# Kernel tuning notes

Measured on AMD Instinct MI355X. Metric: run time of the kernel, lower is better.

The kernel has to match this reference:

```python
import jax, jax.numpy as jnp
import numpy as np
import math

HID = 128      # hidden_dim == d_inner (expand=1)
NSTATE = 8     # d_state
K = 4          # scan directions
RANK = math.ceil(HID / 16)  # dt_rank = 8
B, H, W = 4, 64, 64


def _ln(x, g, b, eps=1e-5):
    m = jnp.mean(x, -1, keepdims=True)
    v = jnp.mean((x - m) ** 2, -1, keepdims=True)
    return (x - m) * jax.lax.rsqrt(v + eps) * g + b


def _ss2d(x, in_w, conv_w, conv_b, xproj_w, dt_w, dt_b, A_logs, Ds, ln_g, ln_b, out_w):
    # x: [B,H,W,C] -> VMamba SS2D with d_inner=C, 4-direction selective scan
    Bn, Hh, Ww, C = x.shape
    D, L = C, Hh * Ww
    N = A_logs.shape[-1]
    R = dt_w.shape[-1]
    xz = x @ in_w.T                      # [B,H,W,2D]
    xc, z = jnp.split(xz, 2, axis=-1)
    xc = xc.transpose(0, 3, 1, 2)        # [B,D,H,W]
    xc = jax.lax.conv_general_dilated(xc, conv_w, (1, 1), 'SAME', feature_group_count=D)
    xc = jax.nn.silu(xc + conv_b[None, :, None, None])
    x_hw = xc.reshape(Bn, D, L)
    x_wh = xc.transpose(0, 1, 3, 2).reshape(Bn, D, L)
    xs = jnp.stack([x_hw, x_wh, x_hw[..., ::-1], x_wh[..., ::-1]], 1)  # [B,K,D,L]
    x_dbl = jnp.einsum('bkdl,kcd->bkcl', xs, xproj_w)
    dts, Bs, Cs = x_dbl[:, :, :R], x_dbl[:, :, R:R + N], x_dbl[:, :, R + N:]
    dt = jax.nn.softplus(jnp.einsum('bkrl,kdr->bkdl', dts, dt_w) + dt_b[None, :, :, None])
    A = -jnp.exp(A_logs.reshape(K, D, N))  # [K,D,N]

    def step(h, inp):
        x_t, dt_t, B_t, C_t = inp          # [B,K,D],[B,K,D],[B,K,N],[B,K,N]
        h = h * jnp.exp(dt_t[..., None] * A) + dt_t[..., None] * B_t[:, :, None, :] * x_t[..., None]
        return h, jnp.einsum('bkdn,bkn->bkd', h, C_t)

    h0 = jnp.zeros((Bn, K, D, N), x.dtype)
    _, ys = jax.lax.scan(step, h0, (xs.transpose(3, 0, 1, 2), dt.transpose(3, 0, 1, 2),
                                    Bs.transpose(3, 0, 1, 2), Cs.transpose(3, 0, 1, 2)))
    out_y = ys.transpose(1, 2, 3, 0) + Ds.reshape(K, D)[None, :, :, None] * xs  # [B,K,D,L]
    wh_y = out_y[:, 3, :, ::-1].reshape(Bn, D, Ww, Hh).transpose(0, 1, 3, 2).reshape(Bn, D, L)
    invwh_y = out_y[:, 1].reshape(Bn, D, Ww, Hh).transpose(0, 1, 3, 2).reshape(Bn, D, L)
    y = out_y[:, 0] + out_y[:, 2, :, ::-1] + wh_y + invwh_y
    y = _ln(y.transpose(0, 2, 1).reshape(Bn, Hh, Ww, D), ln_g, ln_b)
    return (y * jax.nn.silu(z)) @ out_w.T


def _enhance(x, g, b, w, bias):
    return jax.nn.gelu(_ln(x, g, b) @ w.T + bias, approximate=False)


def setup_inputs() -> dict:
    key = jax.random.key(0)
    ks = jax.random.split(key, 12)
    f = lambda k, s, sc=0.02: jax.random.normal(k, s, jnp.float32) * sc
    return dict(
        sar_feat=jax.random.normal(ks[0], (B, H, W, HID), jnp.float32),
        opt_feat=jax.random.normal(ks[1], (B, H, W, HID), jnp.float32),
        ss_in_w=f(ks[2], (2, 2 * HID, HID)),
        ss_conv_w=f(ks[3], (2, HID, 1, 3, 3), 0.1),
        ss_conv_b=f(ks[4], (2, HID)),
        ss_xproj_w=f(ks[5], (2, K, RANK + 2 * NSTATE, HID)),
        ss_dt_w=f(ks[6], (2, K, HID, RANK), 0.1),
        ss_dt_b=f(ks[7], (2, K, HID), 0.1),
        ss_Alogs=jnp.tile(jnp.log(jnp.arange(1, NSTATE + 1, dtype=jnp.float32)), (2, K * HID, 1)),
        ss_Ds=jnp.ones((2, K * HID), jnp.float32),
        ss_ln_g=jnp.ones((2, HID), jnp.float32),
        ss_ln_b=jnp.zeros((2, HID), jnp.float32),
        ss_out_w=f(ks[8], (2, HID, HID)),
        enh_ln_g=jnp.ones((2, HID), jnp.float32),
        enh_ln_b=jnp.zeros((2, HID), jnp.float32),
        enh_w=f(ks[9], (2, HID, HID)),
        enh_b=jnp.zeros((2, HID), jnp.float32),
    )


def reference(sar_feat, opt_feat, ss_in_w, ss_conv_w, ss_conv_b, ss_xproj_w, ss_dt_w,
              ss_dt_b, ss_Alogs, ss_Ds, ss_ln_g, ss_ln_b, ss_out_w,
              enh_ln_g, enh_ln_b, enh_w, enh_b):
    # cat([opt,sar],-1)[...,:C] == opt ; cat([sar,opt],-1)[...,:C] == sar (faithful identity slice)
    # index 0 = cross_ss2d_s2o (input opt), index 1 = cross_ss2d_o2s (input sar)
    xin = jnp.stack([opt_feat, sar_feat])
    guided = jax.vmap(_ss2d)(xin, ss_in_w, ss_conv_w, ss_conv_b, ss_xproj_w, ss_dt_w,
                             ss_dt_b, ss_Alogs, ss_Ds, ss_ln_g, ss_ln_b, ss_out_w)
    # enhance params: index 0 = enhance_sar (on sar_guided=guided[1]), index 1 = enhance_opt (on opt_guided=guided[0])
    enh_in = jnp.stack([guided[1], guided[0]])
    enhanced = jax.vmap(_enhance)(enh_in, enh_ln_g, enh_ln_b, enh_w, enh_b)
    return (sar_feat + enhanced[0], opt_feat + enhanced[1])
```

## Files before the change

kernel.cpp:

```cpp
#include <hip/hip_runtime.h>
#include <hip/hip_bf16.h>
#include <math.h>

#define DEV __device__ __forceinline__

static constexpr int LL = 4096;
static constexpr int DD = 128;
static constexpr int SEG = 64;
static constexpr float LOG2E = 1.4426950408889634f;
static constexpr float LN2 = 0.6931471805599453f;

template <bool B> struct BoolT { static constexpr bool value = B; };

DEV float silu_(float x) { return x / (1.f + __expf(-x)); }
DEV float gelu_(float x) { return 0.5f * x * (1.f + erff(x * 0.7071067811865475f)); }
DEV float sp_(float x) {
  const float t = __builtin_amdgcn_exp2f(-fabsf(x) * LOG2E);
  return fmaxf(x, 0.f) + LN2 * __builtin_amdgcn_logf(1.f + t);
}

template <int CTRL>
DEV float dpp_add_(float x) {
  int y = __builtin_amdgcn_update_dpp(0, __float_as_int(x), CTRL, 0xF, 0xF, true);
  return x + __int_as_float(y);
}

DEV void seg_base_step(int k, int s, int& base, int& step) {
  if (k == 0)      { base = s * 64;        step = 1;   }
  else if (k == 1) { base = s;             step = 64;  }
  else if (k == 2) { base = 4095 - s * 64; step = -1;  }
  else             { base = 4095 - s;      step = -64; }
}

__global__ __launch_bounds__(256) void k_inproj(
    const float* __restrict__ sar, const float* __restrict__ opt,
    const float* __restrict__ in_w, float* __restrict__ xz) {
  const int lt = blockIdx.x, ct = blockIdx.y, mb = blockIdx.z;
  const int m = mb >> 2;
  const float* __restrict__ x = (m == 0 ? opt : sar) + (size_t)(mb & 3) * (LL * DD);
  const float* __restrict__ W = in_w + (size_t)m * 256 * DD;
  __shared__ float sA[64][68];
  __shared__ float sW[64][68];
  const int tid = threadIdx.x;
  const int tc = tid & 15, tl = tid >> 4;
  float acc[4][4] = {};
  for (int db = 0; db < 2; ++db) {
    __syncthreads();
    for (int idx = tid; idx < 64 * 16; idx += 256) {
      const int r = idx >> 4, d4 = (idx & 15) << 2;
      *(float4*)&sA[r][d4] = *(const float4*)&x[(size_t)(lt * 64 + r) * DD + db * 64 + d4];
      *(float4*)&sW[r][d4] = *(const float4*)&W[(size_t)(ct * 64 + r) * DD + db * 64 + d4];
    }
    __syncthreads();
#pragma unroll 4
    for (int d = 0; d < 64; d += 4) {
      float4 a[4], w[4];
#pragma unroll
      for (int q = 0; q < 4; ++q) a[q] = *(const float4*)&sA[tl * 4 + q][d];
#pragma unroll
      for (int j = 0; j < 4; ++j) w[j] = *(const float4*)&sW[tc + 16 * j][d];
#pragma unroll
      for (int j = 0; j < 4; ++j)
#pragma unroll
        for (int q = 0; q < 4; ++q)
          acc[j][q] += a[q].x * w[j].x + a[q].y * w[j].y + a[q].z * w[j].z + a[q].w * w[j].w;
    }
  }
  float* __restrict__ dst = xz + ((size_t)mb * 256 + ct * 64) * LL + lt * 64;
#pragma unroll
  for (int j = 0; j < 4; ++j) {
    float4 v = make_float4(acc[j][0], acc[j][1], acc[j][2], acc[j][3]);
    *(float4*)&dst[(size_t)(tc + 16 * j) * LL + tl * 4] = v;
  }
}

__global__ __launch_bounds__(256) void k_conv(
    const float* __restrict__ xz, const float* __restrict__ conv_w,
    const float* __restrict__ conv_b, float* __restrict__ xc) {
  const int ht = blockIdx.x, dg = blockIdx.y, mb = blockIdx.z;
  const int m = mb >> 2;
  __shared__ float sIn[8][18][66];
  __shared__ float sOut[1024][8];
  const float* __restrict__ src = xz + ((size_t)mb * 256 + dg * 8) * LL;
  const int tid = threadIdx.x;
  for (int idx = tid; idx < 8 * 18 * 66; idx += 256) {
    const int dd = idx / (18 * 66);
    const int rem = idx - dd * (18 * 66);
    const int hh = rem / 66, ww = rem - hh * 66;
    const int h = ht * 16 + hh - 1, w = ww - 1;
    float v = 0.f;
    if (h >= 0 && h < 64 && w >= 0 && w < 64) v = src[(size_t)dd * LL + h * 64 + w];
    sIn[dd][hh][ww] = v;
  }
  __syncthreads();
  const int dd = tid & 7, wv = tid >> 3;
  const int dch = dg * 8 + dd;
  float wk[9];
#pragma unroll
  for (int t = 0; t < 9; ++t) wk[t] = conv_w[((size_t)m * DD + dch) * 9 + t];
  const float bias = conv_b[m * DD + dch];
  for (int hh = 0; hh < 16; ++hh) {
#pragma unroll
    for (int wh = 0; wh < 2; ++wh) {
      const int w = wv + wh * 32;
      float s = bias;
#pragma unroll
      for (int kh = 0; kh < 3; ++kh)
#pragma unroll
        for (int kw = 0; kw < 3; ++kw)
          s = fmaf(sIn[dd][hh + kh][w + kw], wk[kh * 3 + kw], s);
      sOut[hh * 64 + w][dd] = silu_(s);
    }
  }
  __syncthreads();
  float* __restrict__ dst = xc + (size_t)mb * LL * DD + dg * 8;
#pragma unroll
  for (int r = 0; r < 4; ++r) {
    const int pos = tid + r * 256;
    const int l = ht * 1024 + pos;
    *(float4*)&dst[(size_t)l * DD + 0] = *(const float4*)&sOut[pos][0];
    *(float4*)&dst[(size_t)l * DD + 4] = *(const float4*)&sOut[pos][4];
  }
}

__global__ __launch_bounds__(256) void k_xproj(
    const float* __restrict__ xc, const float* __restrict__ xproj_w,
    float* __restrict__ xdbl) {
  const int lt = blockIdx.x, k = blockIdx.y, mb = blockIdx.z;
  const int m = mb >> 2, mbk = mb * 4 + k;
  __shared__ float sX[64][132];
  __shared__ float sW[24][132];
  const int tid = threadIdx.x;
  const float* __restrict__ src = xc + (size_t)mb * LL * DD;
  int base, step;
  seg_base_step(k, lt, base, step);
  for (int idx = tid; idx < 64 * 32; idx += 256) {
    const int l = idx >> 5, d4 = (idx & 31) << 2;
    *(float4*)&sX[l][d4] = *(const float4*)&src[(size_t)(base + l * step) * DD + d4];
  }
  const float* __restrict__ Wsrc = xproj_w + ((size_t)m * 4 + k) * 24 * DD;
  for (int idx = tid; idx < 24 * 32; idx += 256) {
    const int r = idx >> 5, d4 = (idx & 31) << 2;
    *(float4*)&sW[r][d4] = *(const float4*)&Wsrc[(size_t)r * DD + d4];
  }
  __syncthreads();
  const int l = tid >> 2, cg = tid & 3;
  float acc[6] = {};
#pragma unroll 8
  for (int d = 0; d < 128; d += 4) {
    const float4 xv = *(const float4*)&sX[l][d];
#pragma unroll
    for (int j = 0; j < 6; ++j) {
      const float4 wv = *(const float4*)&sW[cg * 6 + j][d];
      acc[j] += xv.x * wv.x + xv.y * wv.y + xv.z * wv.z + xv.w * wv.w;
    }
  }
  float* __restrict__ dst = xdbl + ((size_t)mbk * LL + lt * 64 + l) * 24 + cg * 6;
#pragma unroll
  for (int j = 0; j < 6; ++j) dst[j] = acc[j];
}


__global__ __launch_bounds__(128) void k_scan1(
    const float* __restrict__ xc, const float* __restrict__ xdbl,
    const float* __restrict__ dt_w, const float* __restrict__ dt_b,
    const float* __restrict__ Alogs, float* __restrict__ hend,
    float* __restrict__ Pseg) {
  const int seg = blockIdx.x;
  const int k = blockIdx.y, mb = blockIdx.z;
  const int m = mb >> 2, mbk = mb * 4 + k;
  const int d = threadIdx.x;
  __shared__ float slds[64 * 24];

  float aln2[8];
  {
    const float4 a0 = *(const float4*)&Alogs[((size_t)m * 512 + k * DD + d) * 8];
    const float4 a1 = *(const float4*)&Alogs[((size_t)m * 512 + k * DD + d) * 8 + 4];
    aln2[0] = -__expf(a0.x) * LOG2E; aln2[1] = -__expf(a0.y) * LOG2E;
    aln2[2] = -__expf(a0.z) * LOG2E; aln2[3] = -__expf(a0.w) * LOG2E;
    aln2[4] = -__expf(a1.x) * LOG2E; aln2[5] = -__expf(a1.y) * LOG2E;
    aln2[6] = -__expf(a1.z) * LOG2E; aln2[7] = -__expf(a1.w) * LOG2E;
  }
  bool fastp = true;
#pragma unroll
  for (int n = 1; n < 8; ++n)
    fastp = fastp && (fabsf(aln2[n] - (float)(n + 1) * aln2[0]) <=
                      1e-4f * fabsf(aln2[n]) + 1e-12f);
  float wreg[8];
  {
    const float4 w0 = *(const float4*)&dt_w[((size_t)mbk * DD + d) * 8];
    const float4 w1 = *(const float4*)&dt_w[((size_t)mbk * DD + d) * 8 + 4];
    wreg[0] = w0.x; wreg[1] = w0.y; wreg[2] = w0.z; wreg[3] = w0.w;
    wreg[4] = w1.x; wreg[5] = w1.y; wreg[6] = w1.z; wreg[7] = w1.w;
  }
  const float bw = dt_b[(size_t)mbk * DD + d];

  const float* __restrict__ tsrc = xdbl + ((size_t)mbk * LL + seg * 64) * 24;
#pragma unroll
  for (int t = 0; t < 3; ++t) {
    const int idx = d + t * 128;
    ((float4*)slds)[idx] = ((const float4*)tsrc)[idx];
  }

  int base, step;
  seg_base_step(k, seg, base, step);
  const float* __restrict__ xsrc = xc + (size_t)mb * LL * DD + (size_t)base * DD + d;
  const ptrdiff_t sstep = (ptrdiff_t)step * DD;

  float xreg[8];
#pragma unroll
  for (int j = 0; j < 8; ++j) xreg[j] = xsrc[(ptrdiff_t)j * sstep];
  __syncthreads();

  float h[8] = {0.f, 0.f, 0.f, 0.f, 0.f, 0.f, 0.f, 0.f};
  float dtsum = 0.f;

  auto body = [&](auto ft) {
    constexpr bool F = decltype(ft)::value;
#pragma unroll
    for (int i = 0; i < 64; ++i) {
      const float x = xreg[i & 7];
      if (i + 8 < 64) xreg[i & 7] = xsrc[(ptrdiff_t)(i + 8) * sstep];
      const float4 t0 = *(const float4*)&slds[i * 24 + 0];
      const float4 t1 = *(const float4*)&slds[i * 24 + 4];
      float s = bw;
      s = fmaf(t0.x, wreg[0], s); s = fmaf(t0.y, wreg[1], s);
      s = fmaf(t0.z, wreg[2], s); s = fmaf(t0.w, wreg[3], s);
      s = fmaf(t1.x, wreg[4], s); s = fmaf(t1.y, wreg[5], s);
      s = fmaf(t1.z, wreg[6], s); s = fmaf(t1.w, wreg[7], s);
      const float dt = sp_(s);
      const float u = dt * x;
      dtsum += dt;
      float q1, q2, q3, q4, q5, q6, q7, q8;
      if constexpr (F) {
        q1 = __builtin_amdgcn_exp2f(dt * aln2[0]);
        q2 = q1 * q1; q3 = q2 * q1; q4 = q2 * q2;
        q5 = q4 * q1; q6 = q4 * q2; q7 = q4 * q3; q8 = q4 * q4;
      } else {
        q1 = __builtin_amdgcn_exp2f(dt * aln2[0]);
        q2 = __builtin_amdgcn_exp2f(dt * aln2[1]);
        q3 = __builtin_amdgcn_exp2f(dt * aln2[2]);
        q4 = __builtin_amdgcn_exp2f(dt * aln2[3]);
        q5 = __builtin_amdgcn_exp2f(dt * aln2[4]);
        q6 = __builtin_amdgcn_exp2f(dt * aln2[5]);
        q7 = __builtin_amdgcn_exp2f(dt * aln2[6]);
        q8 = __builtin_amdgcn_exp2f(dt * aln2[7]);
      }
      const float4 b0 = *(const float4*)&slds[i * 24 + 8];
      const float4 b1 = *(const float4*)&slds[i * 24 + 12];
      h[0] = fmaf(h[0], q1, u * b0.x);
      h[1] = fmaf(h[1], q2, u * b0.y);
      h[2] = fmaf(h[2], q3, u * b0.z);
      h[3] = fmaf(h[3], q4, u * b0.w);
      h[4] = fmaf(h[4], q5, u * b1.x);
      h[5] = fmaf(h[5], q6, u * b1.y);
      h[6] = fmaf(h[6], q7, u * b1.z);
      h[7] = fmaf(h[7], q8, u * b1.w);
    }
  };
  if (fastp) body(BoolT<true>{}); else body(BoolT<false>{});

  float* __restrict__ he = hend + (((size_t)mbk * SEG + seg) << 10) + d * 8;
  float* __restrict__ pe = Pseg + (((size_t)mbk * SEG + seg) << 10) + d * 8;
  *(float4*)&he[0] = make_float4(h[0], h[1], h[2], h[3]);
  *(float4*)&he[4] = make_float4(h[4], h[5], h[6], h[7]);
  *(float4*)&pe[0] = make_float4(
      __builtin_amdgcn_exp2f(aln2[0] * dtsum), __builtin_amdgcn_exp2f(aln2[1] * dtsum),
      __builtin_amdgcn_exp2f(aln2[2] * dtsum), __builtin_amdgcn_exp2f(aln2[3] * dtsum));
  *(float4*)&pe[4] = make_float4(
      __builtin_amdgcn_exp2f(aln2[4] * dtsum), __builtin_amdgcn_exp2f(aln2[5] * dtsum),
      __builtin_amdgcn_exp2f(aln2[6] * dtsum), __builtin_amdgcn_exp2f(aln2[7] * dtsum));
}

__global__ __launch_bounds__(256) void k_scan2(
    const float* __restrict__ hend, const float* __restrict__ Pseg,
    float* __restrict__ hin) {
  const int gid = blockIdx.x * 256 + threadIdx.x;
  const int mbk = gid >> 10, dn = gid & 1023;
  const float* __restrict__ P = Pseg + ((size_t)mbk << 16) + dn;
  const float* __restrict__ E = hend + ((size_t)mbk << 16) + dn;
  float* __restrict__ O = hin + ((size_t)mbk << 16) + dn;
  float h = 0.f;
#pragma unroll
  for (int s = 0; s < SEG; ++s) {
    O[(size_t)s << 10] = h;
    if (s < SEG - 1) h = fmaf(P[(size_t)s << 10], h, E[(size_t)s << 10]);
  }
}

__global__ __launch_bounds__(128) void k_scan3(
    const float* __restrict__ xc, const float* __restrict__ xdbl,
    const float* __restrict__ dt_w, const float* __restrict__ dt_b,
    const float* __restrict__ Alogs, const float* __restrict__ Ds,
    const float* __restrict__ hin, float* __restrict__ ysum) {
  const int seg = blockIdx.x;
  const int k = blockIdx.y, mb = blockIdx.z;
  const int m = mb >> 2, mbk = mb * 4 + k;
  const int d = threadIdx.x;
  __shared__ float slds[64 * 24];

  float aln2[8];
  {
    const float4 a0 = *(const float4*)&Alogs[((size_t)m * 512 + k * DD + d) * 8];
    const float4 a1 = *(const float4*)&Alogs[((size_t)m * 512 + k * DD + d) * 8 + 4];
    aln2[0] = -__expf(a0.x) * LOG2E; aln2[1] = -__expf(a0.y) * LOG2E;
    aln2[2] = -__expf(a0.z) * LOG2E; aln2[3] = -__expf(a0.w) * LOG2E;
    aln2[4] = -__expf(a1.x) * LOG2E; aln2[5] = -__expf(a1.y) * LOG2E;
    aln2[6] = -__expf(a1.z) * LOG2E; aln2[7] = -__expf(a1.w) * LOG2E;
  }
  bool fastp = true;
#pragma unroll
  for (int n = 1; n < 8; ++n)
    fastp = fastp && (fabsf(aln2[n] - (float)(n + 1) * aln2[0]) <=
                      1e-4f * fabsf(aln2[n]) + 1e-12f);
  float wreg[8];
  {
    const float4 w0 = *(const float4*)&dt_w[((size_t)mbk * DD + d) * 8];
    const float4 w1 = *(const float4*)&dt_w[((size_t)mbk * DD + d) * 8 + 4];
    wreg[0] = w0.x; wreg[1] = w0.y; wreg[2] = w0.z; wreg[3] = w0.w;
    wreg[4] = w1.x; wreg[5] = w1.y; wreg[6] = w1.z; wreg[7] = w1.w;
  }
  const float bw = dt_b[(size_t)mbk * DD + d];
  const float dsv = Ds[(size_t)m * 512 + k * DD + d];

  const float* __restrict__ tsrc = xdbl + ((size_t)mbk * LL + seg * 64) * 24;
#pragma unroll
  for (int t = 0; t < 3; ++t) {
    const int idx = d + t * 128;
    ((float4*)slds)[idx] = ((const float4*)tsrc)[idx];
  }

  int base, step;
  seg_base_step(k, seg, base, step);
  const float* __restrict__ xsrc = xc + (size_t)mb * LL * DD + (size_t)base * DD + d;
  float* __restrict__ ydst = ysum + (size_t)mb * LL * DD + (size_t)base * DD + d;
  const ptrdiff_t sstep = (ptrdiff_t)step * DD;

  float xreg[8];
#pragma unroll
  for (int j = 0; j < 8; ++j) xreg[j] = xsrc[(ptrdiff_t)j * sstep];

  float h[8];
  {
    const float* __restrict__ hp = hin + (((size_t)mbk * SEG + seg) << 10) + d * 8;
    const float4 h0 = *(const float4*)&hp[0];
    const float4 h1 = *(const float4*)&hp[4];
    h[0] = h0.x; h[1] = h0.y; h[2] = h0.z; h[3] = h0.w;
    h[4] = h1.x; h[5] = h1.y; h[6] = h1.z; h[7] = h1.w;
  }
  __syncthreads();

  auto body = [&](auto ft) {
    constexpr bool F = decltype(ft)::value;
#pragma unroll
    for (int i = 0; i < 64; ++i) {
      const float x = xreg[i & 7];
      if (i + 8 < 64) xreg[i & 7] = xsrc[(ptrdiff_t)(i + 8) * sstep];
      const float4 t0 = *(const float4*)&slds[i * 24 + 0];
      const float4 t1 = *(const float4*)&slds[i * 24 + 4];
      float s = bw;
      s = fmaf(t0.x, wreg[0], s); s = fmaf(t0.y, wreg[1], s);
      s = fmaf(t0.z, wreg[2], s); s = fmaf(t0.w, wreg[3], s);
      s = fmaf(t1.x, wreg[4], s); s = fmaf(t1.y, wreg[5], s);
      s = fmaf(t1.z, wreg[6], s); s = fmaf(t1.w, wreg[7], s);
      const float dt = sp_(s);
      const float u = dt * x;
      float q1, q2, q3, q4, q5, q6, q7, q8;
      if constexpr (F) {
        q1 = __builtin_amdgcn_exp2f(dt * aln2[0]);
        q2 = q1 * q1; q3 = q2 * q1; q4 = q2 * q2;
        q5 = q4 * q1; q6 = q4 * q2; q7 = q4 * q3; q8 = q4 * q4;
      } else {
        q1 = __builtin_amdgcn_exp2f(dt * aln2[0]);
        q2 = __builtin_amdgcn_exp2f(dt * aln2[1]);
        q3 = __builtin_amdgcn_exp2f(dt * aln2[2]);
        q4 = __builtin_amdgcn_exp2f(dt * aln2[3]);
        q5 = __builtin_amdgcn_exp2f(dt * aln2[4]);
        q6 = __builtin_amdgcn_exp2f(dt * aln2[5]);
        q7 = __builtin_amdgcn_exp2f(dt * aln2[6]);
        q8 = __builtin_amdgcn_exp2f(dt * aln2[7]);
      }
      const float4 b0 = *(const float4*)&slds[i * 24 + 8];
      const float4 b1 = *(const float4*)&slds[i * 24 + 12];
      const float4 c0 = *(const float4*)&slds[i * 24 + 16];
      const float4 c1 = *(const float4*)&slds[i * 24 + 20];
      float y = dsv * x;
      h[0] = fmaf(h[0], q1, u * b0.x); y = fmaf(h[0], c0.x, y);
      h[1] = fmaf(h[1], q2, u * b0.y); y = fmaf(h[1], c0.y, y);
      h[2] = fmaf(h[2], q3, u * b0.z); y = fmaf(h[2], c0.z, y);
      h[3] = fmaf(h[3], q4, u * b0.w); y = fmaf(h[3], c0.w, y);
      h[4] = fmaf(h[4], q5, u * b1.x); y = fmaf(h[4], c1.x, y);
      h[5] = fmaf(h[5], q6, u * b1.y); y = fmaf(h[5], c1.y, y);
      h[6] = fmaf(h[6], q7, u * b1.z); y = fmaf(h[6], c1.z, y);
      h[7] = fmaf(h[7], q8, u * b1.w); y = fmaf(h[7], c1.w, y);
      unsafeAtomicAdd(ydst + (ptrdiff_t)i * sstep, y);
    }
  };
  if (fastp) body(BoolT<true>{}); else body(BoolT<false>{});
}

__global__ __launch_bounds__(256) void k_outproj(
    const float* __restrict__ ysum, const float* __restrict__ xz,
    const float* __restrict__ ln_g, const float* __restrict__ ln_b,
    const float* __restrict__ out_w, float* __restrict__ guided) {
  const int lt = blockIdx.x, mb = blockIdx.y;
  const int m = mb >> 2;
  __shared__ float sv[32][132];
  __shared__ float sW[64][68];
  __shared__ float smr[32][2];
  __shared__ float sg[128], sb[128];
  const int tid = threadIdx.x;
  if (tid < 128) { sg[tid] = ln_g[m * DD + tid]; sb[tid] = ln_b[m * DD + tid]; }
  const float4* __restrict__ ysrc = (const float4*)(ysum + ((size_t)mb * LL + lt * 32) * DD);
  for (int idx = tid; idx < 1024; idx += 256)
    *(float4*)&sv[idx >> 5][(idx & 31) << 2] = ysrc[idx];
  __syncthreads();
  {
    const int l = tid >> 3, q = tid & 7;
    float s = 0.f, s2 = 0.f;
#pragma unroll
    for (int d0 = 0; d0 < 16; d0 += 4) {
      const float4 v = *(const float4*)&sv[l][q * 16 + d0];
      s += v.x + v.y + v.z + v.w;
      s2 += v.x * v.x + v.y * v.y + v.z * v.z + v.w * v.w;
    }
    s = dpp_add_<0xB1>(s); s = dpp_add_<0x4E>(s); s = dpp_add_<0x141>(s);
    s2 = dpp_add_<0xB1>(s2); s2 = dpp_add_<0x4E>(s2); s2 = dpp_add_<0x141>(s2);
    if (q == 0) {
      const float mean = s * (1.f / 128.f);
      smr[l][0] = mean;
      smr[l][1] = rsqrtf(fmaf(s2, 1.f / 128.f, -mean * mean) + 1e-5f);
    }
  }
  __syncthreads();
  {
    const int c = tid >> 1, half = tid & 1;
    const float* __restrict__ zsrc = xz + ((size_t)mb * 256 + 128 + c) * LL + lt * 32 + half * 16;
    const float g = sg[c], bb = sb[c];
#pragma unroll
    for (int i = 0; i < 16; i += 4) {
      const float4 z4 = *(const float4*)&zsrc[i];
      const float zz[4] = {z4.x, z4.y, z4.z, z4.w};
#pragma unroll
      for (int t = 0; t < 4; ++t) {
        const int l = half * 16 + i + t;
        const float v = fmaf((sv[l][c] - smr[l][0]) * smr[l][1], g, bb);
        sv[l][c] = v * silu_(zz[t]);
      }
    }
  }
  const int tc = tid & 15, tl = tid >> 4;
  const float* __restrict__ Wp = out_w + (size_t)m * DD * DD;
  float* __restrict__ dst = guided + ((size_t)mb * LL + lt * 32) * DD;
  for (int jb = 0; jb < 2; ++jb) {
    float acc[4][2] = {};
    for (int db = 0; db < 2; ++db) {
      __syncthreads();
      for (int idx = tid; idx < 64 * 16; idx += 256) {
        const int r = idx >> 4, d4 = (idx & 15) << 2;
        *(float4*)&sW[r][d4] = *(const float4*)&Wp[(size_t)(jb * 64 + r) * DD + db * 64 + d4];
      }
      __syncthreads();
#pragma unroll 4
      for (int d0 = 0; d0 < 64; d0 += 4) {
        float4 av[2], wv[4];
#pragma unroll
        for (int q = 0; q < 2; ++q) av[q] = *(const float4*)&sv[tl * 2 + q][db * 64 + d0];
#pragma unroll
        for (int j = 0; j < 4; ++j) wv[j] = *(const float4*)&sW[tc + 16 * j][d0];
#pragma unroll
        for (int j = 0; j < 4; ++j)
#pragma unroll
          for (int q = 0; q < 2; ++q)
            acc[j][q] += av[q].x * wv[j].x + av[q].y * wv[j].y + av[q].z * wv[j].z + av[q].w * wv[j].w;
      }
    }
#pragma unroll
    for (int j = 0; j < 4; ++j)
#pragma unroll
      for (int q = 0; q < 2; ++q)
        dst[(size_t)(tl * 2 + q) * DD + jb * 64 + tc + 16 * j] = acc[j][q];
  }
}

__global__ __launch_bounds__(256) void k_enhance(
    const float* __restrict__ guided, const float* __restrict__ eg,
    const float* __restrict__ ebv, const float* __restrict__ ew,
    const float* __restrict__ ebias, const float* __restrict__ sar,
    const float* __restrict__ opt, float* __restrict__ outp) {
  const int lt = blockIdx.x, ib = blockIdx.y;
  const int i = ib >> 2, b = ib & 3;
  __shared__ float sv[32][132];
  __shared__ float sW[64][68];
  __shared__ float smr[32][2];
  __shared__ float sg[128], sb2[128], sbias[128];
  const int tid = threadIdx.x;
  if (tid < 128) {
    sg[tid] = eg[i * DD + tid];
    sb2[tid] = ebv[i * DD + tid];
    sbias[tid] = ebias[i * DD + tid];
  }
  const float4* __restrict__ gsrc =
      (const float4*)(guided + (((size_t)(1 - i) * 4 + b) * LL + lt * 32) * DD);
  for (int idx = tid; idx < 1024; idx += 256)
    *(float4*)&sv[idx >> 5][(idx & 31) << 2] = gsrc[idx];
  __syncthreads();
  {
    const int l = tid >> 3, q = tid & 7;
    float s = 0.f, s2 = 0.f;
#pragma unroll
    for (int d0 = 0; d0 < 16; d0 += 4) {
      const float4 v = *(const float4*)&sv[l][q * 16 + d0];
      s += v.x + v.y + v.z + v.w;
      s2 += v.x * v.x + v.y * v.y + v.z * v.z + v.w * v.w;
    }
    s = dpp_add_<0xB1>(s); s = dpp_add_<0x4E>(s); s = dpp_add_<0x141>(s);
    s2 = dpp_add_<0xB1>(s2); s2 = dpp_add_<0x4E>(s2); s2 = dpp_add_<0x141>(s2);
    if (q == 0) {
      const float mean = s * (1.f / 128.f);
      smr[l][0] = mean;
      smr[l][1] = rsqrtf(fmaf(s2, 1.f / 128.f, -mean * mean) + 1e-5f);
    }
  }
  __syncthreads();
  {
    const int c = tid >> 1, half = tid & 1;
    const float g = sg[c], bb = sb2[c];
#pragma unroll
    for (int i2 = 0; i2 < 16; ++i2) {
      const int l = half * 16 + i2;
      sv[l][c] = fmaf((sv[l][c] - smr[l][0]) * smr[l][1], g, bb);
    }
  }
  const int tc = tid & 15, tl = tid >> 4;
  const float* __restrict__ Wp = ew + (size_t)i * DD * DD;
  const float* __restrict__ resid = (i == 0 ? sar : opt) + ((size_t)b * LL + lt * 32) * DD;
  float* __restrict__ dst = outp + (size_t)i * (4 * LL * DD) + ((size_t)b * LL + lt * 32) * DD;
  for (int jb = 0; jb < 2; ++jb) {
    float acc[4][2] = {};
    for (int db = 0; db < 2; ++db) {
      __syncthreads();
      for (int idx = tid; idx < 64 * 16; idx += 256) {
        const int r = idx >> 4, d4 = (idx & 15) << 2;
        *(float4*)&sW[r][d4] = *(const float4*)&Wp[(size_t)(jb * 64 + r) * DD + db * 64 + d4];
      }
      __syncthreads();
#pragma unroll 4
      for (int d0 = 0; d0 < 64; d0 += 4) {
        float4 av[2], wv[4];
#pragma unroll
        for (int q = 0; q < 2; ++q) av[q] = *(const float4*)&sv[tl * 2 + q][db * 64 + d0];
#pragma unroll
        for (int j = 0; j < 4; ++j) wv[j] = *(const float4*)&sW[tc + 16 * j][d0];
#pragma unroll
        for (int j = 0; j < 4; ++j)
#pragma unroll
          for (int q = 0; q < 2; ++q)
            acc[j][q] += av[q].x * wv[j].x + av[q].y * wv[j].y + av[q].z * wv[j].z + av[q].w * wv[j].w;
      }
    }
#pragma unroll
    for (int j = 0; j < 4; ++j)
#pragma unroll
      for (int q = 0; q < 2; ++q) {
        const int col = jb * 64 + tc + 16 * j;
        const int row = tl * 2 + q;
        const float u = acc[j][q] + sbias[col];
        dst[(size_t)row * DD + col] = resid[(size_t)row * DD + col] + gelu_(u);
      }
  }
}

extern "C" void kernel_launch(void* const* d_in, const int* in_sizes, int n_in,
                              void* d_out, int out_size, void* d_ws, size_t ws_size,
                              hipStream_t stream) {
  (void)in_sizes; (void)n_in; (void)out_size; (void)ws_size;
  const float* sar    = (const float*)d_in[0];
  const float* opt    = (const float*)d_in[1];
  const float* in_w   = (const float*)d_in[2];
  const float* conv_w = (const float*)d_in[3];
  const float* conv_b = (const float*)d_in[4];
  const float* xproj_w= (const float*)d_in[5];
  const float* dt_w   = (const float*)d_in[6];
  const float* dt_b   = (const float*)d_in[7];
  const float* Alogs  = (const float*)d_in[8];
  const float* Ds     = (const float*)d_in[9];
  const float* ln_g   = (const float*)d_in[10];
  const float* ln_b   = (const float*)d_in[11];
  const float* out_w  = (const float*)d_in[12];
  const float* eg     = (const float*)d_in[13];
  const float* eb     = (const float*)d_in[14];
  const float* ew     = (const float*)d_in[15];
  const float* ebias  = (const float*)d_in[16];

  float* ws     = (float*)d_ws;
  float* xz     = ws;
  float* xc     = xz + 8388608;
  float* xdbl   = xc + 4194304;
  float* ysumb  = xdbl + 3145728;
  float* guided = ysumb + 4194304;
  float* hend   = guided + 4194304;
  float* Pseg   = hend + 2097152;
  float* hin    = Pseg + 2097152;
  float* outf   = (float*)d_out;

  hipMemsetAsync(ysumb, 0, (size_t)4194304 * sizeof(float), stream);
  k_inproj <<<dim3(64, 4, 8), 256, 0, stream>>>(sar, opt, in_w, xz);
  k_conv   <<<dim3(4, 16, 8), 256, 0, stream>>>(xz, conv_w, conv_b, xc);
  k_xproj  <<<dim3(64, 4, 8), 256, 0, stream>>>(xc, xproj_w, xdbl);
  k_scan1  <<<dim3(63, 4, 8), 128, 0, stream>>>(xc, xdbl, dt_w, dt_b, Alogs, hend, Pseg);
  k_scan2  <<<dim3(128), 256, 0, stream>>>(hend, Pseg, hin);
  k_scan3  <<<dim3(64, 4, 8), 128, 0, stream>>>(xc, xdbl, dt_w, dt_b, Alogs, Ds, hin, ysumb);
  k_outproj<<<dim3(128, 8), 256, 0, stream>>>(ysumb, xz, ln_g, ln_b, out_w, guided);
  k_enhance<<<dim3(128, 8), 256, 0, stream>>>(guided, eg, eb, ew, ebias, sar, opt, outf);
}
```

Before: 290.2 us.

## Pair forward/reverse scan directions per block, drop atomic ysum and memset

Each scan block now handles a forward direction and its reversed counterpart over the same physical positions. The pair shares x loads, and scan3 combines the two outputs through an LDS buffer and writes them with plain stores to separate row and column buffers. This removes the memset and the previous accumulation into a single ysum array. The out-projection sums the two buffers. The out-projection and enhance kernels also prefetch weight tiles into registers, and GELU now uses a polynomial erf approximation. In exchange the scan grid is halved, LDS use per block rises (32KB ybuf), and the erf approximation adds a small numerical error.

```diff
diff --git a/kernel.cpp b/kernel.cpp
--- a/kernel.cpp
+++ b/kernel.cpp
@@ -10,10 +10,19 @@
 static constexpr float LOG2E = 1.4426950408889634f;
 static constexpr float LN2 = 0.6931471805599453f;
 
-template <bool B> struct BoolT { static constexpr bool value = B; };
-
 DEV float silu_(float x) { return x / (1.f + __expf(-x)); }
-DEV float gelu_(float x) { return 0.5f * x * (1.f + erff(x * 0.7071067811865475f)); }
+DEV float erf_(float x) {
+  const float ax = fabsf(x);
+  const float t = 1.f / fmaf(0.3275911f, ax, 1.f);
+  float p = fmaf(1.061405429f, t, -1.453152027f);
+  p = fmaf(p, t, 1.421413741f);
+  p = fmaf(p, t, -0.284496736f);
+  p = fmaf(p, t, 0.254829592f);
+  p = p * t;
+  const float r = 1.f - p * __expf(-ax * ax);
+  return x < 0.f ? -r : r;
+}
+DEV float gelu_(float x) { return 0.5f * x * (1.f + erf_(x * 0.7071067811865475f)); }
 DEV float sp_(float x) {
   const float t = __builtin_amdgcn_exp2f(-fabsf(x) * LOG2E);
   return fmaxf(x, 0.f) + LN2 * __builtin_amdgcn_logf(1.f + t);
@@ -161,115 +170,209 @@
 }
 
 
+template <bool REV, bool FAST>
+DEV void scan1_dir(const float* __restrict__ slds, const float* __restrict__ xs0,
+                   ptrdiff_t sstep, const float* __restrict__ aln2,
+                   const float* __restrict__ wreg, float bw,
+                   float* __restrict__ h, float& dtsum) {
+  float xreg[8];
+#pragma unroll
+  for (int t = 0; t < 8; ++t)
+    xreg[t] = xs0[(ptrdiff_t)(REV ? 63 - t : t) * sstep];
+#pragma unroll 8
+  for (int j = 0; j < 64; ++j) {
+    const float x = xreg[j & 7];
+    if (j + 8 < 64) xreg[j & 7] = xs0[(ptrdiff_t)(REV ? 55 - j : j + 8) * sstep];
+    const float4 t0 = *(const float4*)&slds[j * 24 + 0];
+    const float4 t1 = *(const float4*)&slds[j * 24 + 4];
+    float s = bw;
+    s = fmaf(t0.x, wreg[0], s); s = fmaf(t0.y, wreg[1], s);
+    s = fmaf(t0.z, wreg[2], s); s = fmaf(t0.w, wreg[3], s);
+    s = fmaf(t1.x, wreg[4], s); s = fmaf(t1.y, wreg[5], s);
+    s = fmaf(t1.z, wreg[6], s); s = fmaf(t1.w, wreg[7], s);
+    const float dt = sp_(s);
+    const float u = dt * x;
+    dtsum += dt;
+    float q1, q2, q3, q4, q5, q6, q7, q8;
+    if constexpr (FAST) {
+      q1 = __builtin_amdgcn_exp2f(dt * aln2[0]);
+      q2 = q1 * q1; q3 = q2 * q1; q4 = q2 * q2;
+      q5 = q4 * q1; q6 = q4 * q2; q7 = q4 * q3; q8 = q4 * q4;
+    } else {
+      q1 = __builtin_amdgcn_exp2f(dt * aln2[0]);
+      q2 = __builtin_amdgcn_exp2f(dt * aln2[1]);
+      q3 = __builtin_amdgcn_exp2f(dt * aln2[2]);
+      q4 = __builtin_amdgcn_exp2f(dt * aln2[3]);
+      q5 = __builtin_amdgcn_exp2f(dt * aln2[4]);
+      q6 = __builtin_amdgcn_exp2f(dt * aln2[5]);
+      q7 = __builtin_amdgcn_exp2f(dt * aln2[6]);
+      q8 = __builtin_amdgcn_exp2f(dt * aln2[7]);
+    }
+    const float4 b0 = *(const float4*)&slds[j * 24 + 8];
+    const float4 b1 = *(const float4*)&slds[j * 24 + 12];
+    h[0] = fmaf(h[0], q1, u * b0.x);
+    h[1] = fmaf(h[1], q2, u * b0.y);
+    h[2] = fmaf(h[2], q3, u * b0.z);
+    h[3] = fmaf(h[3], q4, u * b0.w);
+    h[4] = fmaf(h[4], q5, u * b1.x);
+    h[5] = fmaf(h[5], q6, u * b1.y);
+    h[6] = fmaf(h[6], q7, u * b1.z);
+    h[7] = fmaf(h[7], q8, u * b1.w);
+  }
+}
+
+template <bool REV, bool FAST>
+DEV void scan3_dir(const float* __restrict__ slds, const float* __restrict__ xs0,
+                   ptrdiff_t sstep, const float* __restrict__ aln2,
+                   const float* __restrict__ wreg, float bw, float dsv,
+                   float* __restrict__ h, float* __restrict__ ybuf,
+                   float* __restrict__ yd0, int d) {
+  float xreg[8];
+#pragma unroll
+  for (int t = 0; t < 8; ++t)
+    xreg[t] = xs0[(ptrdiff_t)(REV ? 63 - t : t) * sstep];
+#pragma unroll 8
+  for (int j = 0; j < 64; ++j) {
+    const int phys = REV ? 63 - j : j;
+    const float x = xreg[j & 7];
+    if (j + 8 < 64) xreg[j & 7] = xs0[(ptrdiff_t)(REV ? 55 - j : j + 8) * sstep];
+    const float4 t0 = *(const float4*)&slds[j * 24 + 0];
+    const float4 t1 = *(const float4*)&slds[j * 24 + 4];
+    float s = bw;
+    s = fmaf(t0.x, wreg[0], s); s = fmaf(t0.y, wreg[1], s);
+    s = fmaf(t0.z, wreg[2], s); s = fmaf(t0.w, wreg[3], s);
+    s = fmaf(t1.x, wreg[4], s); s = fmaf(t1.y, wreg[5], s);
+    s = fmaf(t1.z, wreg[6], s); s = fmaf(t1.w, wreg[7], s);
+    const float dt = sp_(s);
+    const float u = dt * x;
+    float q1, q2, q3, q4, q5, q6, q7, q8;
+    if constexpr (FAST) {
+      q1 = __builtin_amdgcn_exp2f(dt * aln2[0]);
+      q2 = q1 * q1; q3 = q2 * q1; q4 = q2 * q2;
+      q5 = q4 * q1; q6 = q4 * q2; q7 = q4 * q3; q8 = q4 * q4;
+    } else {
+      q1 = __builtin_amdgcn_exp2f(dt * aln2[0]);
+      q2 = __builtin_amdgcn_exp2f(dt * aln2[1]);
+      q3 = __builtin_amdgcn_exp2f(dt * aln2[2]);
+      q4 = __builtin_amdgcn_exp2f(dt * aln2[3]);
+      q5 = __builtin_amdgcn_exp2f(dt * aln2[4]);
+      q6 = __builtin_amdgcn_exp2f(dt * aln2[5]);
+      q7 = __builtin_amdgcn_exp2f(dt * aln2[6]);
+      q8 = __builtin_amdgcn_exp2f(dt * aln2[7]);
+    }
+    const float4 b0 = *(const float4*)&slds[j * 24 + 8];
+    const float4 b1 = *(const float4*)&slds[j * 24 + 12];
+    const float4 c0 = *(const float4*)&slds[j * 24 + 16];
+    const float4 c1 = *(const float4*)&slds[j * 24 + 20];
+    float y = dsv * x;
+    h[0] = fmaf(h[0], q1, u * b0.x); y = fmaf(h[0], c0.x, y);
+    h[1] = fmaf(h[1], q2, u * b0.y); y = fmaf(h[1], c0.y, y);
+    h[2] = fmaf(h[2], q3, u * b0.z); y = fmaf(h[2], c0.z, y);
+    h[3] = fmaf(h[3], q4, u * b0.w); y = fmaf(h[3], c0.w, y);
+    h[4] = fmaf(h[4], q5, u * b1.x); y = fmaf(h[4], c1.x, y);
+    h[5] = fmaf(h[5], q6, u * b1.y); y = fmaf(h[5], c1.y, y);
+    h[6] = fmaf(h[6], q7, u * b1.z); y = fmaf(h[6], c1.z, y);
+    h[7] = fmaf(h[7], q8, u * b1.w); y = fmaf(h[7], c1.w, y);
+    if constexpr (REV) {
+      yd0[(ptrdiff_t)phys * sstep] = y + ybuf[phys * 128 + d];
+    } else {
+      ybuf[j * 128 + d] = y;
+    }
+  }
+}
+
+DEV void load_aln2(const float* __restrict__ Alogs, int m, int k, int d,
+                   float* __restrict__ aln2, bool& fastp) {
+  const float4 a0 = *(const float4*)&Alogs[((size_t)m * 512 + k * DD + d) * 8];
+  const float4 a1 = *(const float4*)&Alogs[((size_t)m * 512 + k * DD + d) * 8 + 4];
+  aln2[0] = -__expf(a0.x) * LOG2E; aln2[1] = -__expf(a0.y) * LOG2E;
+  aln2[2] = -__expf(a0.z) * LOG2E; aln2[3] = -__expf(a0.w) * LOG2E;
+  aln2[4] = -__expf(a1.x) * LOG2E; aln2[5] = -__expf(a1.y) * LOG2E;
+  aln2[6] = -__expf(a1.z) * LOG2E; aln2[7] = -__expf(a1.w) * LOG2E;
+  fastp = true;
+#pragma unroll
+  for (int n = 1; n < 8; ++n)
+    fastp = fastp && (fabsf(aln2[n] - (float)(n + 1) * aln2[0]) <=
+                      1e-4f * fabsf(aln2[n]) + 1e-12f);
+}
+
+DEV void load_w8(const float* __restrict__ dt_w, int mbk, int d,
+                 float* __restrict__ wreg) {
+  const float4 w0 = *(const float4*)&dt_w[((size_t)mbk * DD + d) * 8];
+  const float4 w1 = *(const float4*)&dt_w[((size_t)mbk * DD + d) * 8 + 4];
+  wreg[0] = w0.x; wreg[1] = w0.y; wreg[2] = w0.z; wreg[3] = w0.w;
+  wreg[4] = w1.x; wreg[5] = w1.y; wreg[6] = w1.z; wreg[7] = w1.w;
+}
+
 __global__ __launch_bounds__(128) void k_scan1(
     const float* __restrict__ xc, const float* __restrict__ xdbl,
     const float* __restrict__ dt_w, const float* __restrict__ dt_b,
     const float* __restrict__ Alogs, float* __restrict__ hend,
     float* __restrict__ Pseg) {
-  const int seg = blockIdx.x;
-  const int k = blockIdx.y, mb = blockIdx.z;
-  const int m = mb >> 2, mbk = mb * 4 + k;
+  const int s = blockIdx.x, p = blockIdx.y, mb = blockIdx.z;
+  const int m = mb >> 2;
+  const int kA = p, kB = p + 2;
+  const int segA = s, segB = 63 - s;
+  const int mbkA = mb * 4 + kA, mbkB = mb * 4 + kB;
   const int d = threadIdx.x;
-  __shared__ float slds[64 * 24];
-
-  float aln2[8];
+  __shared__ float sldsA[64 * 24], sldsB[64 * 24];
+
+  const float4* tA = (const float4*)(xdbl + ((size_t)mbkA * LL + segA * 64) * 24);
+  const float4* tB = (const float4*)(xdbl + ((size_t)mbkB * LL + segB * 64) * 24);
+#pragma unroll
+  for (int t = 0; t < 3; ++t) {
+    ((float4*)sldsA)[d + t * 128] = tA[d + t * 128];
+    ((float4*)sldsB)[d + t * 128] = tB[d + t * 128];
+  }
+
+  const int base0 = (p == 0) ? s * 64 : s;
+  const int stepPos = (p == 0) ? 1 : 64;
+  const ptrdiff_t sstep = (ptrdiff_t)stepPos * DD;
+  const float* __restrict__ xs0 = xc + (size_t)mb * LL * DD + (size_t)base0 * DD + d;
+  __syncthreads();
+
   {
-    const float4 a0 = *(const float4*)&Alogs[((size_t)m * 512 + k * DD + d) * 8];
-    const float4 a1 = *(const float4*)&Alogs[((size_t)m * 512 + k * DD + d) * 8 + 4];
-    aln2[0] = -__expf(a0.x) * LOG2E; aln2[1] = -__expf(a0.y) * LOG2E;
-    aln2[2] = -__expf(a0.z) * LOG2E; aln2[3] = -__expf(a0.w) * LOG2E;
-    aln2[4] = -__expf(a1.x) * LOG2E; aln2[5] = -__expf(a1.y) * LOG2E;
-    aln2[6] = -__expf(a1.z) * LOG2E; aln2[7] = -__expf(a1.w) * LOG2E;
-  }
-  bool fastp = true;
-#pragma unroll
-  for (int n = 1; n < 8; ++n)
-    fastp = fastp && (fabsf(aln2[n] - (float)(n + 1) * aln2[0]) <=
-                      1e-4f * fabsf(aln2[n]) + 1e-12f);
-  float wreg[8];
+    float aln2[8]; bool fastp;
+    load_aln2(Alogs, m, kA, d, aln2, fastp);
+    float wreg[8];
+    load_w8(dt_w, mbkA, d, wreg);
+    const float bw = dt_b[(size_t)mbkA * DD + d];
+    float h[8] = {0, 0, 0, 0, 0, 0, 0, 0};
+    float dtsum = 0.f;
+    if (fastp) scan1_dir<false, true>(sldsA, xs0, sstep, aln2, wreg, bw, h, dtsum);
+    else       scan1_dir<false, false>(sldsA, xs0, sstep, aln2, wreg, bw, h, dtsum);
+    float* __restrict__ he = hend + (((size_t)mbkA * SEG + segA) << 10) + d * 8;
+    float* __restrict__ pe = Pseg + (((size_t)mbkA * SEG + segA) << 10) + d * 8;
+    *(float4*)&he[0] = make_float4(h[0], h[1], h[2], h[3]);
+    *(float4*)&he[4] = make_float4(h[4], h[5], h[6], h[7]);
+    *(float4*)&pe[0] = make_float4(
+        __builtin_amdgcn_exp2f(aln2[0] * dtsum), __builtin_amdgcn_exp2f(aln2[1] * dtsum),
+        __builtin_amdgcn_exp2f(aln2[2] * dtsum), __builtin_amdgcn_exp2f(aln2[3] * dtsum));
+    *(float4*)&pe[4] = make_float4(
+        __builtin_amdgcn_exp2f(aln2[4] * dtsum), __builtin_amdgcn_exp2f(aln2[5] * dtsum),
+        __builtin_amdgcn_exp2f(aln2[6] * dtsum), __builtin_amdgcn_exp2f(aln2[7] * dtsum));
+  }
   {
-    const float4 w0 = *(const float4*)&dt_w[((size_t)mbk * DD + d) * 8];
-    const float4 w1 = *(const float4*)&dt_w[((size_t)mbk * DD + d) * 8 + 4];
-    wreg[0] = w0.x; wreg[1] = w0.y; wreg[2] = w0.z; wreg[3] = w0.w;
-    wreg[4] = w1.x; wreg[5] = w1.y; wreg[6] = w1.z; wreg[7] = w1.w;
-  }
-  const float bw = dt_b[(size_t)mbk * DD + d];
-
-  const float* __restrict__ tsrc = xdbl + ((size_t)mbk * LL + seg * 64) * 24;
-#pragma unroll
-  for (int t = 0; t < 3; ++t) {
-    const int idx = d + t * 128;
-    ((float4*)slds)[idx] = ((const float4*)tsrc)[idx];
-  }
-
-  int base, step;
-  seg_base_step(k, seg, base, step);
-  const float* __restrict__ xsrc = xc + (size_t)mb * LL * DD + (size_t)base * DD + d;
-  const ptrdiff_t sstep = (ptrdiff_t)step * DD;
-
-  float xreg[8];
-#pragma unroll
-  for (int j = 0; j < 8; ++j) xreg[j] = xsrc[(ptrdiff_t)j * sstep];
-  __syncthreads();
-
-  float h[8] = {0.f, 0.f, 0.f, 0.f, 0.f, 0.f, 0.f, 0.f};
-  float dtsum = 0.f;
-
-  auto body = [&](auto ft) {
-    constexpr bool F = decltype(ft)::value;
-#pragma unroll
-    for (int i = 0; i < 64; ++i) {
-      const float x = xreg[i & 7];
-      if (i + 8 < 64) xreg[i & 7] = xsrc[(ptrdiff_t)(i + 8) * sstep];
-      const float4 t0 = *(const float4*)&slds[i * 24 + 0];
-      const float4 t1 = *(const float4*)&slds[i * 24 + 4];
-      float s = bw;
-      s = fmaf(t0.x, wreg[0], s); s = fmaf(t0.y, wreg[1], s);
-      s = fmaf(t0.z, wreg[2], s); s = fmaf(t0.w, wreg[3], s);
-      s = fmaf(t1.x, wreg[4], s); s = fmaf(t1.y, wreg[5], s);
-      s = fmaf(t1.z, wreg[6], s); s = fmaf(t1.w, wreg[7], s);
-      const float dt = sp_(s);
-      const float u = dt * x;
-      dtsum += dt;
-      float q1, q2, q3, q4, q5, q6, q7, q8;
-      if constexpr (F) {
-        q1 = __builtin_amdgcn_exp2f(dt * aln2[0]);
-        q2 = q1 * q1; q3 = q2 * q1; q4 = q2 * q2;
-        q5 = q4 * q1; q6 = q4 * q2; q7 = q4 * q3; q8 = q4 * q4;
-      } else {
-        q1 = __builtin_amdgcn_exp2f(dt * aln2[0]);
-        q2 = __builtin_amdgcn_exp2f(dt * aln2[1]);
-        q3 = __builtin_amdgcn_exp2f(dt * aln2[2]);
-        q4 = __builtin_amdgcn_exp2f(dt * aln2[3]);
-        q5 = __builtin_amdgcn_exp2f(dt * aln2[4]);
-        q6 = __builtin_amdgcn_exp2f(dt * aln2[5]);
-        q7 = __builtin_amdgcn_exp2f(dt * aln2[6]);
-        q8 = __builtin_amdgcn_exp2f(dt * aln2[7]);
-      }
-      const float4 b0 = *(const float4*)&slds[i * 24 + 8];
-      const float4 b1 = *(const float4*)&slds[i * 24 + 12];
-      h[0] = fmaf(h[0], q1, u * b0.x);
-      h[1] = fmaf(h[1], q2, u * b0.y);
-      h[2] = fmaf(h[2], q3, u * b0.z);
-      h[3] = fmaf(h[3], q4, u * b0.w);
-      h[4] = fmaf(h[4], q5, u * b1.x);
-      h[5] = fmaf(h[5], q6, u * b1.y);
-      h[6] = fmaf(h[6], q7, u * b1.z);
-      h[7] = fmaf(h[7], q8, u * b1.w);
-    }
-  };
-  if (fastp) body(BoolT<true>{}); else body(BoolT<false>{});
-
-  float* __restrict__ he = hend + (((size_t)mbk * SEG + seg) << 10) + d * 8;
-  float* __restrict__ pe = Pseg + (((size_t)mbk * SEG + seg) << 10) + d * 8;
-  *(float4*)&he[0] = make_float4(h[0], h[1], h[2], h[3]);
-  *(float4*)&he[4] = make_float4(h[4], h[5], h[6], h[7]);
-  *(float4*)&pe[0] = make_float4(
-      __builtin_amdgcn_exp2f(aln2[0] * dtsum), __builtin_amdgcn_exp2f(aln2[1] * dtsum),
-      __builtin_amdgcn_exp2f(aln2[2] * dtsum), __builtin_amdgcn_exp2f(aln2[3] * dtsum));
-  *(float4*)&pe[4] = make_float4(
-      __builtin_amdgcn_exp2f(aln2[4] * dtsum), __builtin_amdgcn_exp2f(aln2[5] * dtsum),
-      __builtin_amdgcn_exp2f(aln2[6] * dtsum), __builtin_amdgcn_exp2f(aln2[7] * dtsum));
+    float aln2[8]; bool fastp;
+    load_aln2(Alogs, m, kB, d, aln2, fastp);
+    float wreg[8];
+    load_w8(dt_w, mbkB, d, wreg);
+    const float bw = dt_b[(size_t)mbkB * DD + d];
+    float h[8] = {0, 0, 0, 0, 0, 0, 0, 0};
+    float dtsum = 0.f;
+    if (fastp) scan1_dir<true, true>(sldsB, xs0, sstep, aln2, wreg, bw, h, dtsum);
+    else       scan1_dir<true, false>(sldsB, xs0, sstep, aln2, wreg, bw, h, dtsum);
+    float* __restrict__ he = hend + (((size_t)mbkB * SEG + segB) << 10) + d * 8;
+    float* __restrict__ pe = Pseg + (((size_t)mbkB * SEG + segB) << 10) + d * 8;
+    *(float4*)&he[0] = make_float4(h[0], h[1], h[2], h[3]);
+    *(float4*)&he[4] = make_float4(h[4], h[5], h[6], h[7]);
+    *(float4*)&pe[0] = make_float4(
+        __builtin_amdgcn_exp2f(aln2[0] * dtsum), __builtin_amdgcn_exp2f(aln2[1] * dtsum),
+        __builtin_amdgcn_exp2f(aln2[2] * dtsum), __builtin_amdgcn_exp2f(aln2[3] * dtsum));
+    *(float4*)&pe[4] = make_float4(
+        __builtin_amdgcn_exp2f(aln2[4] * dtsum), __builtin_amdgcn_exp2f(aln2[5] * dtsum),
+        __builtin_amdgcn_exp2f(aln2[6] * dtsum), __builtin_amdgcn_exp2f(aln2[7] * dtsum));
+  }
 }
 
 __global__ __launch_bounds__(256) void k_scan2(
@@ -292,117 +395,76 @@
     const float* __restrict__ xc, const float* __restrict__ xdbl,
     const float* __restrict__ dt_w, const float* __restrict__ dt_b,
     const float* __restrict__ Alogs, const float* __restrict__ Ds,
-    const float* __restrict__ hin, float* __restrict__ ysum) {
-  const int seg = blockIdx.x;
-  const int k = blockIdx.y, mb = blockIdx.z;
-  const int m = mb >> 2, mbk = mb * 4 + k;
+    const float* __restrict__ hin, float* __restrict__ yrow,
+    float* __restrict__ ycol) {
+  const int s = blockIdx.x, p = blockIdx.y, mb = blockIdx.z;
+  const int m = mb >> 2;
+  const int kA = p, kB = p + 2;
+  const int segA = s, segB = 63 - s;
+  const int mbkA = mb * 4 + kA, mbkB = mb * 4 + kB;
   const int d = threadIdx.x;
-  __shared__ float slds[64 * 24];
-
-  float aln2[8];
+  __shared__ float sldsA[64 * 24], sldsB[64 * 24];
+  __shared__ float ybuf[64 * 128];
+
+  const float4* tA = (const float4*)(xdbl + ((size_t)mbkA * LL + segA * 64) * 24);
+  const float4* tB = (const float4*)(xdbl + ((size_t)mbkB * LL + segB * 64) * 24);
+#pragma unroll
+  for (int t = 0; t < 3; ++t) {
+    ((float4*)sldsA)[d + t * 128] = tA[d + t * 128];
+    ((float4*)sldsB)[d + t * 128] = tB[d + t * 128];
+  }
+
+  const int base0 = (p == 0) ? s * 64 : s;
+  const int stepPos = (p == 0) ? 1 : 64;
+  const ptrdiff_t sstep = (ptrdiff_t)stepPos * DD;
+  const float* __restrict__ xs0 = xc + (size_t)mb * LL * DD + (size_t)base0 * DD + d;
+  float* __restrict__ yd0 =
+      (p == 0 ? yrow : ycol) + (size_t)mb * LL * DD + (size_t)base0 * DD + d;
+  __syncthreads();
+
   {
-    const float4 a0 = *(const float4*)&Alogs[((size_t)m * 512 + k * DD + d) * 8];
-    const float4 a1 = *(const float4*)&Alogs[((size_t)m * 512 + k * DD + d) * 8 + 4];
-    aln2[0] = -__expf(a0.x) * LOG2E; aln2[1] = -__expf(a0.y) * LOG2E;
-    aln2[2] = -__expf(a0.z) * LOG2E; aln2[3] = -__expf(a0.w) * LOG2E;
-    aln2[4] = -__expf(a1.x) * LOG2E; aln2[5] = -__expf(a1.y) * LOG2E;
-    aln2[6] = -__expf(a1.z) * LOG2E; aln2[7] = -__expf(a1.w) * LOG2E;
-  }
-  bool fastp = true;
-#pragma unroll
-  for (int n = 1; n < 8; ++n)
-    fastp = fastp && (fabsf(aln2[n] - (float)(n + 1) * aln2[0]) <=
-                      1e-4f * fabsf(aln2[n]) + 1e-12f);
-  float wreg[8];
+    float aln2[8]; bool fastp;
+    load_aln2(Alogs, m, kA, d, aln2, fastp);
+    float wreg[8];
+    load_w8(dt_w, mbkA, d, wreg);
+    const float bw = dt_b[(size_t)mbkA * DD + d];
+    const float dsv = Ds[(size_t)m * 512 + kA * DD + d];
+    float h[8];
+    {
+      const float* hp = hin + (((size_t)mbkA * SEG + segA) << 10) + d * 8;
+      const float4 h0 = *(const float4*)&hp[0];
+      const float4 h1 = *(const float4*)&hp[4];
+      h[0] = h0.x; h[1] = h0.y; h[2] = h0.z; h[3] = h0.w;
+      h[4] = h1.x; h[5] = h1.y; h[6] = h1.z; h[7] = h1.w;
+    }
+    if (fastp) scan3_dir<false, true>(sldsA, xs0, sstep, aln2, wreg, bw, dsv, h, ybuf, yd0, d);
+    else       scan3_dir<false, false>(sldsA, xs0, sstep, aln2, wreg, bw, dsv, h, ybuf, yd0, d);
+  }
   {
-    const float4 w0 = *(const float4*)&dt_w[((size_t)mbk * DD + d) * 8];
-    const float4 w1 = *(const float4*)&dt_w[((size_t)mbk * DD + d) * 8 + 4];
-    wreg[0] = w0.x; wreg[1] = w0.y; wreg[2] = w0.z; wreg[3] = w0.w;
-    wreg[4] = w1.x; wreg[5] = w1.y; wreg[6] = w1.z; wreg[7] = w1.w;
-  }
-  const float bw = dt_b[(size_t)mbk * DD + d];
-  const float dsv = Ds[(size_t)m * 512 + k * DD + d];
-
-  const float* __restrict__ tsrc = xdbl + ((size_t)mbk * LL + seg * 64) * 24;
-#pragma unroll
-  for (int t = 0; t < 3; ++t) {
-    const int idx = d + t * 128;
-    ((float4*)slds)[idx] = ((const float4*)tsrc)[idx];
-  }
-
-  int base, step;
-  seg_base_step(k, seg, base, step);
-  const float* __restrict__ xsrc = xc + (size_t)mb * LL * DD + (size_t)base * DD + d;
-  float* __restrict__ ydst = ysum + (size_t)mb * LL * DD + (size_t)base * DD + d;
-  const ptrdiff_t sstep = (ptrdiff_t)step * DD;
-
-  float xreg[8];
-#pragma unroll
-  for (int j = 0; j < 8; ++j) xreg[j] = xsrc[(ptrdiff_t)j * sstep];
-
-  float h[8];
-  {
-    const float* __restrict__ hp = hin + (((size_t)mbk * SEG + seg) << 10) + d * 8;
-    const float4 h0 = *(const float4*)&hp[0];
-    const float4 h1 = *(const float4*)&hp[4];
-    h[0] = h0.x; h[1] = h0.y; h[2] = h0.z; h[3] = h0.w;
-    h[4] = h1.x; h[5] = h1.y; h[6] = h1.z; h[7] = h1.w;
-  }
-  __syncthreads();
-
-  auto body = [&](auto ft) {
-    constexpr bool F = decltype(ft)::value;
-#pragma unroll
-    for (int i = 0; i < 64; ++i) {
-      const float x = xreg[i & 7];
-      if (i + 8 < 64) xreg[i & 7] = xsrc[(ptrdiff_t)(i + 8) * sstep];
-      const float4 t0 = *(const float4*)&slds[i * 24 + 0];
-      const float4 t1 = *(const float4*)&slds[i * 24 + 4];
-      float s = bw;
-      s = fmaf(t0.x, wreg[0], s); s = fmaf(t0.y, wreg[1], s);
-      s = fmaf(t0.z, wreg[2], s); s = fmaf(t0.w, wreg[3], s);
-      s = fmaf(t1.x, wreg[4], s); s = fmaf(t1.y, wreg[5], s);
-      s = fmaf(t1.z, wreg[6], s); s = fmaf(t1.w, wreg[7], s);
-      const float dt = sp_(s);
-      const float u = dt * x;
-      float q1, q2, q3, q4, q5, q6, q7, q8;
-      if constexpr (F) {
-        q1 = __builtin_amdgcn_exp2f(dt * aln2[0]);
-        q2 = q1 * q1; q3 = q2 * q1; q4 = q2 * q2;
-        q5 = q4 * q1; q6 = q4 * q2; q7 = q4 * q3; q8 = q4 * q4;
-      } else {
-        q1 = __builtin_amdgcn_exp2f(dt * aln2[0]);
-        q2 = __builtin_amdgcn_exp2f(dt * aln2[1]);
-        q3 = __builtin_amdgcn_exp2f(dt * aln2[2]);
-        q4 = __builtin_amdgcn_exp2f(dt * aln2[3]);
-        q5 = __builtin_amdgcn_exp2f(dt * aln2[4]);
-        q6 = __builtin_amdgcn_exp2f(dt * aln2[5]);
-        q7 = __builtin_amdgcn_exp2f(dt * aln2[6]);
-        q8 = __builtin_amdgcn_exp2f(dt * aln2[7]);
-      }
-      const float4 b0 = *(const float4*)&slds[i * 24 + 8];
-      const float4 b1 = *(const float4*)&slds[i * 24 + 12];
-      const float4 c0 = *(const float4*)&slds[i * 24 + 16];
-      const float4 c1 = *(const float4*)&slds[i * 24 + 20];
-      float y = dsv * x;
-      h[0] = fmaf(h[0], q1, u * b0.x); y = fmaf(h[0], c0.x, y);
-      h[1] = fmaf(h[1], q2, u * b0.y); y = fmaf(h[1], c0.y, y);
-      h[2] = fmaf(h[2], q3, u * b0.z); y = fmaf(h[2], c0.z, y);
-      h[3] = fmaf(h[3], q4, u * b0.w); y = fmaf(h[3], c0.w, y);
-      h[4] = fmaf(h[4], q5, u * b1.x); y = fmaf(h[4], c1.x, y);
-      h[5] = fmaf(h[5], q6, u * b1.y); y = fmaf(h[5], c1.y, y);
-      h[6] = fmaf(h[6], q7, u * b1.z); y = fmaf(h[6], c1.z, y);
-      h[7] = fmaf(h[7], q8, u * b1.w); y = fmaf(h[7], c1.w, y);
-      unsafeAtomicAdd(ydst + (ptrdiff_t)i * sstep, y);
-    }
-  };
-  if (fastp) body(BoolT<true>{}); else body(BoolT<false>{});
+    float aln2[8]; bool fastp;
+    load_aln2(Alogs, m, kB, d, aln2, fastp);
+    float wreg[8];
+    load_w8(dt_w, mbkB, d, wreg);
+    const float bw = dt_b[(size_t)mbkB * DD + d];
+    const float dsv = Ds[(size_t)m * 512 + kB * DD + d];
+    float h[8];
+    {
+      const float* hp = hin + (((size_t)mbkB * SEG + segB) << 10) + d * 8;
+      const float4 h0 = *(const float4*)&hp[0];
+      const float4 h1 = *(const float4*)&hp[4];
+      h[0] = h0.x; h[1] = h0.y; h[2] = h0.z; h[3] = h0.w;
+      h[4] = h1.x; h[5] = h1.y; h[6] = h1.z; h[7] = h1.w;
+    }
+    if (fastp) scan3_dir<true, true>(sldsB, xs0, sstep, aln2, wreg, bw, dsv, h, ybuf, yd0, d);
+    else       scan3_dir<true, false>(sldsB, xs0, sstep, aln2, wreg, bw, dsv, h, ybuf, yd0, d);
+  }
 }
 
 __global__ __launch_bounds__(256) void k_outproj(
-    const float* __restrict__ ysum, const float* __restrict__ xz,
-    const float* __restrict__ ln_g, const float* __restrict__ ln_b,
-    const float* __restrict__ out_w, float* __restrict__ guided) {
+    const float* __restrict__ yrow, const float* __restrict__ ycol,
+    const float* __restrict__ xz, const float* __restrict__ ln_g,
+    const float* __restrict__ ln_b, const float* __restrict__ out_w,
+    float* __restrict__ guided) {
   const int lt = blockIdx.x, mb = blockIdx.y;
   const int m = mb >> 2;
   __shared__ float sv[32][132];
@@ -410,10 +472,32 @@
   __shared__ float smr[32][2];
   __shared__ float sg[128], sb[128];
   const int tid = threadIdx.x;
+  const float4* y1 = (const float4*)(yrow + ((size_t)mb * LL + lt * 32) * DD);
+  const float4* y2 = (const float4*)(ycol + ((size_t)mb * LL + lt * 32) * DD);
+  float4 yv[4], yw[4];
+#pragma unroll
+  for (int t = 0; t < 4; ++t) { yv[t] = y1[tid + t * 256]; yw[t] = y2[tid + t * 256]; }
+  const int zc = tid >> 1, zh = tid & 1;
+  const float4* zsrc = (const float4*)(xz + ((size_t)mb * 256 + 128 + zc) * LL + lt * 32 + zh * 16);
+  float4 zv[4];
+#pragma unroll
+  for (int t = 0; t < 4; ++t) zv[t] = zsrc[t];
+  const float* __restrict__ Wp = out_w + (size_t)m * DD * DD;
+  float4 wpre[4];
+#pragma unroll
+  for (int t = 0; t < 4; ++t) {
+    const int idx = tid + t * 256;
+    wpre[t] = *(const float4*)&Wp[(size_t)(idx >> 4) * DD + ((idx & 15) << 2)];
+  }
   if (tid < 128) { sg[tid] = ln_g[m * DD + tid]; sb[tid] = ln_b[m * DD + tid]; }
-  const float4* __restrict__ ysrc = (const float4*)(ysum + ((size_t)mb * LL + lt * 32) * DD);
-  for (int idx = tid; idx < 1024; idx += 256)
-    *(float4*)&sv[idx >> 5][(idx & 31) << 2] = ysrc[idx];
+#pragma unroll
+  for (int t = 0; t < 4; ++t) {
+    const int idx = tid + t * 256;
+    float4 v;
+    v.x = yv[t].x + yw[t].x; v.y = yv[t].y + yw[t].y;
+    v.z = yv[t].z + yw[t].z; v.w = yv[t].w + yw[t].w;
+    *(float4*)&sv[idx >> 5][(idx & 31) << 2] = v;
+  }
   __syncthreads();
   {
     const int l = tid >> 3, q = tid & 7;
@@ -434,31 +518,36 @@
   }
   __syncthreads();
   {
-    const int c = tid >> 1, half = tid & 1;
-    const float* __restrict__ zsrc = xz + ((size_t)mb * 256 + 128 + c) * LL + lt * 32 + half * 16;
-    const float g = sg[c], bb = sb[c];
-#pragma unroll
-    for (int i = 0; i < 16; i += 4) {
-      const float4 z4 = *(const float4*)&zsrc[i];
-      const float zz[4] = {z4.x, z4.y, z4.z, z4.w};
-#pragma unroll
-      for (int t = 0; t < 4; ++t) {
-        const int l = half * 16 + i + t;
-        const float v = fmaf((sv[l][c] - smr[l][0]) * smr[l][1], g, bb);
-        sv[l][c] = v * silu_(zz[t]);
-      }
+    const float g = sg[zc], bb = sb[zc];
+    const float* zf = (const float*)zv;
+#pragma unroll
+    for (int i2 = 0; i2 < 16; ++i2) {
+      const int l = zh * 16 + i2;
+      const float v = fmaf((sv[l][zc] - smr[l][0]) * smr[l][1], g, bb);
+      sv[l][zc] = v * silu_(zf[i2]);
     }
   }
   const int tc = tid & 15, tl = tid >> 4;
-  const float* __restrict__ Wp = out_w + (size_t)m * DD * DD;
   float* __restrict__ dst = guided + ((size_t)mb * LL + lt * 32) * DD;
+#pragma unroll
   for (int jb = 0; jb < 2; ++jb) {
     float acc[4][2] = {};
+#pragma unroll
     for (int db = 0; db < 2; ++db) {
       __syncthreads();
-      for (int idx = tid; idx < 64 * 16; idx += 256) {
-        const int r = idx >> 4, d4 = (idx & 15) << 2;
-        *(float4*)&sW[r][d4] = *(const float4*)&Wp[(size_t)(jb * 64 + r) * DD + db * 64 + d4];
+#pragma unroll
+      for (int t = 0; t < 4; ++t) {
+        const int idx = tid + t * 256;
+        *(float4*)&sW[idx >> 4][(idx & 15) << 2] = wpre[t];
+      }
+      const int ph = jb * 2 + db + 1;
+      if (ph < 4) {
+        const int jb2 = ph >> 1, db2 = ph & 1;
+#pragma unroll
+        for (int t = 0; t < 4; ++t) {
+          const int idx = tid + t * 256;
+          wpre[t] = *(const float4*)&Wp[(size_t)(jb2 * 64 + (idx >> 4)) * DD + db2 * 64 + ((idx & 15) << 2)];
+        }
       }
       __syncthreads();
 #pragma unroll 4
@@ -495,15 +584,28 @@
   __shared__ float smr[32][2];
   __shared__ float sg[128], sb2[128], sbias[128];
   const int tid = threadIdx.x;
+  const float4* gsrc =
+      (const float4*)(guided + (((size_t)(1 - i) * 4 + b) * LL + lt * 32) * DD);
+  float4 gv[4];
+#pragma unroll
+  for (int t = 0; t < 4; ++t) gv[t] = gsrc[tid + t * 256];
+  const float* __restrict__ Wp = ew + (size_t)i * DD * DD;
+  float4 wpre[4];
+#pragma unroll
+  for (int t = 0; t < 4; ++t) {
+    const int idx = tid + t * 256;
+    wpre[t] = *(const float4*)&Wp[(size_t)(idx >> 4) * DD + ((idx & 15) << 2)];
+  }
   if (tid < 128) {
     sg[tid] = eg[i * DD + tid];
     sb2[tid] = ebv[i * DD + tid];
     sbias[tid] = ebias[i * DD + tid];
   }
-  const float4* __restrict__ gsrc =
-      (const float4*)(guided + (((size_t)(1 - i) * 4 + b) * LL + lt * 32) * DD);
-  for (int idx = tid; idx < 1024; idx += 256)
-    *(float4*)&sv[idx >> 5][(idx & 31) << 2] = gsrc[idx];
+#pragma unroll
+  for (int t = 0; t < 4; ++t) {
+    const int idx = tid + t * 256;
+    *(float4*)&sv[idx >> 5][(idx & 31) << 2] = gv[t];
+  }
   __syncthreads();
   {
     const int l = tid >> 3, q = tid & 7;
@@ -533,18 +635,38 @@
     }
   }
   const int tc = tid & 15, tl = tid >> 4;
-  const float* __restrict__ Wp = ew + (size_t)i * DD * DD;
   const float* __restrict__ resid = (i == 0 ? sar : opt) + ((size_t)b * LL + lt * 32) * DD;
   float* __restrict__ dst = outp + (size_t)i * (4 * LL * DD) + ((size_t)b * LL + lt * 32) * DD;
+  float rv[16];
+#pragma unroll
+  for (int jb = 0; jb < 2; ++jb)
+#pragma unroll
+    for (int j = 0; j < 4; ++j)
+#pragma unroll
+      for (int q = 0; q < 2; ++q)
+        rv[jb * 8 + j * 2 + q] = resid[(size_t)(tl * 2 + q) * DD + jb * 64 + tc + 16 * j];
+  float accA[4][2] = {}, accB[4][2] = {};
+#pragma unroll
   for (int jb = 0; jb < 2; ++jb) {
-    float acc[4][2] = {};
+#pragma unroll
     for (int db = 0; db < 2; ++db) {
       __syncthreads();
-      for (int idx = tid; idx < 64 * 16; idx += 256) {
-        const int r = idx >> 4, d4 = (idx & 15) << 2;
-        *(float4*)&sW[r][d4] = *(const float4*)&Wp[(size_t)(jb * 64 + r) * DD + db * 64 + d4];
+#pragma unroll
+      for (int t = 0; t < 4; ++t) {
+        const int idx = tid + t * 256;
+        *(float4*)&sW[idx >> 4][(idx & 15) << 2] = wpre[t];
+      }
+      const int ph = jb * 2 + db + 1;
+      if (ph < 4) {
+        const int jb2 = ph >> 1, db2 = ph & 1;
+#pragma unroll
+        for (int t = 0; t < 4; ++t) {
+          const int idx = tid + t * 256;
+          wpre[t] = *(const float4*)&Wp[(size_t)(jb2 * 64 + (idx >> 4)) * DD + db2 * 64 + ((idx & 15) << 2)];
+        }
       }
       __syncthreads();
+      float (*acc)[2] = (jb == 0) ? accA : accB;
 #pragma unroll 4
       for (int d0 = 0; d0 < 64; d0 += 4) {
         float4 av[2], wv[4];
@@ -559,16 +681,17 @@
             acc[j][q] += av[q].x * wv[j].x + av[q].y * wv[j].y + av[q].z * wv[j].z + av[q].w * wv[j].w;
       }
     }
+  }
+#pragma unroll
+  for (int jb = 0; jb < 2; ++jb)
 #pragma unroll
     for (int j = 0; j < 4; ++j)
 #pragma unroll
       for (int q = 0; q < 2; ++q) {
         const int col = jb * 64 + tc + 16 * j;
-        const int row = tl * 2 + q;
-        const float u = acc[j][q] + sbias[col];
-        dst[(size_t)row * DD + col] = resid[(size_t)row * DD + col] + gelu_(u);
+        const float u = ((jb == 0) ? accA[j][q] : accB[j][q]) + sbias[col];
+        dst[(size_t)(tl * 2 + q) * DD + col] = rv[jb * 8 + j * 2 + q] + gelu_(u);
       }
-  }
 }
 
 extern "C" void kernel_launch(void* const* d_in, const int* in_sizes, int n_in,
@@ -597,20 +720,20 @@
   float* xz     = ws;
   float* xc     = xz + 8388608;
   float* xdbl   = xc + 4194304;
-  float* ysumb  = xdbl + 3145728;
-  float* guided = ysumb + 4194304;
+  float* yrowb  = xdbl + 3145728;
+  float* ycolb  = yrowb + 4194304;
+  float* guided = ycolb + 4194304;
   float* hend   = guided + 4194304;
   float* Pseg   = hend + 2097152;
   float* hin    = Pseg + 2097152;
   float* outf   = (float*)d_out;
 
-  hipMemsetAsync(ysumb, 0, (size_t)4194304 * sizeof(float), stream);
   k_inproj <<<dim3(64, 4, 8), 256, 0, stream>>>(sar, opt, in_w, xz);
   k_conv   <<<dim3(4, 16, 8), 256, 0, stream>>>(xz, conv_w, conv_b, xc);
   k_xproj  <<<dim3(64, 4, 8), 256, 0, stream>>>(xc, xproj_w, xdbl);
-  k_scan1  <<<dim3(63, 4, 8), 128, 0, stream>>>(xc, xdbl, dt_w, dt_b, Alogs, hend, Pseg);
+  k_scan1  <<<dim3(64, 2, 8), 128, 0, stream>>>(xc, xdbl, dt_w, dt_b, Alogs, hend, Pseg);
   k_scan2  <<<dim3(128), 256, 0, stream>>>(hend, Pseg, hin);
-  k_scan3  <<<dim3(64, 4, 8), 128, 0, stream>>>(xc, xdbl, dt_w, dt_b, Alogs, Ds, hin, ysumb);
-  k_outproj<<<dim3(128, 8), 256, 0, stream>>>(ysumb, xz, ln_g, ln_b, out_w, guided);
+  k_scan3  <<<dim3(64, 2, 8), 128, 0, stream>>>(xc, xdbl, dt_w, dt_b, Alogs, Ds, hin, yrowb, ycolb);
+  k_outproj<<<dim3(128, 8), 256, 0, stream>>>(yrowb, ycolb, xz, ln_g, ln_b, out_w, guided);
   k_enhance<<<dim3(128, 8), 256, 0, stream>>>(guided, eg, eb, ew, ebias, sar, opt, outf);
 }
```

New measurement: 326.7 us. +12.6%, slower.
